# Performance work log

Measured on AMD Instinct MI355X. Metric: run time of the kernel, lower is better.

## Reference

```python
import jax, jax.numpy as jnp
import numpy as np

HEADS = 16
DIM_HEAD = 64
LN_EPS = 1e-5


def setup_inputs() -> dict:
    key = jax.random.key(0)
    ks = jax.random.split(key, 4)
    b, n, dim = 2, 2048, 1024
    inner = HEADS * DIM_HEAD
    x = jax.random.normal(ks[0], (b, n, dim), dtype=jnp.float32)
    gamma = jnp.ones((dim,), dtype=jnp.float32)
    beta = jnp.zeros((dim,), dtype=jnp.float32)
    w_qkv = jax.random.normal(ks[1], (dim, 3 * inner), dtype=jnp.float32) * (dim ** -0.5)
    w_out = jax.random.normal(ks[2], (inner, dim), dtype=jnp.float32) * (inner ** -0.5)
    b_out = jnp.zeros((dim,), dtype=jnp.float32)
    return {"x": x, "gamma": gamma, "beta": beta, "w_qkv": w_qkv, "w_out": w_out, "b_out": b_out}


def reference(x, gamma, beta, w_qkv, w_out, b_out):
    b, n, dim = x.shape
    h, d = HEADS, DIM_HEAD
    scale = d ** -0.5
    # LayerNorm
    mu = jnp.mean(x, axis=-1, keepdims=True)
    var = jnp.mean(jnp.square(x - mu), axis=-1, keepdims=True)
    xn = (x - mu) * jax.lax.rsqrt(var + LN_EPS) * gamma + beta
    # QKV projection (no bias)
    qkv = xn @ w_qkv  # [b, n, 3*h*d]
    q, k, v = jnp.split(qkv, 3, axis=-1)
    split_heads = lambda t: t.reshape(b, n, h, d).transpose(0, 2, 1, 3)  # [b, h, n, d]
    q, k, v = split_heads(q), split_heads(k), split_heads(v)
    q = q * scale
    sim = jnp.einsum('bhid,bhjd->bhij', q, k)  # full O(n^2) score matrix
    attn = jax.nn.softmax(sim, axis=-1)
    out = jnp.einsum('bhij,bhjd->bhid', attn, v)
    out = out.transpose(0, 2, 1, 3).reshape(b, n, h * d)
    return out @ w_out + b_out
```

## Files before the change

kernel.cpp:

```cpp
#include <hip/hip_runtime.h>
#include <hip/hip_bf16.h>

#define HEADS 16
#define DH 64
#define DIM 1024
#define SEQ 2048
#define BATCH 2
#define ROWS (BATCH*SEQ)
#define NQKV (3*DIM)
#define NKVT (SEQ/64)
#define NSPLIT 2
#define QSCALE 0.18033688011112042f
#define NBH (BATCH*HEADS)
#define NQROWS (NBH*SEQ)

typedef __attribute__((ext_vector_type(8))) short bf16x8;
typedef __attribute__((ext_vector_type(4))) float f32x4;
typedef __attribute__((ext_vector_type(16))) float f32x16;
typedef __attribute__((ext_vector_type(4))) unsigned u32x4;
typedef __hip_bfloat16 bf16;

static __device__ __forceinline__ bf16 f2bf(float v){ return __float2bfloat16(v); }

static __device__ __forceinline__ unsigned cvtpk(float a, float b){
  unsigned r;
  asm("v_cvt_pk_bf16_f32 %0, %1, %2" : "=v"(r) : "v"(a), "v"(b));
  return r;
}

static __device__ __forceinline__ void gload16(const void* g, void* lds){
  __builtin_amdgcn_global_load_lds((const __attribute__((address_space(1))) void*)g,
                                   (__attribute__((address_space(3))) void*)lds, 16, 0, 0);
}

__global__ __launch_bounds__(256) void prep_kernel(
    const float* __restrict__ x, const float* __restrict__ gamma,
    const float* __restrict__ beta, bf16* __restrict__ xn,
    const float* __restrict__ w_qkv, bf16* __restrict__ wqt,
    const float* __restrict__ w_out, bf16* __restrict__ wot)
{
  __shared__ float red[8];
  __shared__ __align__(16) bf16 tt[64][72];
  int bid = blockIdx.x;
  int tid = threadIdx.x;
  if (bid < ROWS){
    int row = bid;
    float4 v = ((const float4*)(x + (size_t)row*DIM))[tid];
    float s  = v.x+v.y+v.z+v.w;
    float ss = v.x*v.x+v.y*v.y+v.z*v.z+v.w*v.w;
    #pragma unroll
    for (int m=1;m<64;m<<=1){ s += __shfl_xor(s,m); ss += __shfl_xor(ss,m); }
    int wid = tid>>6;
    if ((tid&63)==0){ red[wid]=s; red[4+wid]=ss; }
    __syncthreads();
    s  = red[0]+red[1]+red[2]+red[3];
    ss = red[4]+red[5]+red[6]+red[7];
    float mu  = s*(1.0f/DIM);
    float var = ss*(1.0f/DIM) - mu*mu;
    float inv = rsqrtf(var + 1e-5f);
    float4 g  = ((const float4*)gamma)[tid];
    float4 bb = ((const float4*)beta)[tid];
    __align__(8) bf16 o[4];
    o[0]=f2bf((v.x-mu)*inv*g.x+bb.x);
    o[1]=f2bf((v.y-mu)*inv*g.y+bb.y);
    o[2]=f2bf((v.z-mu)*inv*g.z+bb.z);
    o[3]=f2bf((v.w-mu)*inv*g.w+bb.w);
    *(uint2*)&xn[(size_t)row*DIM + tid*4] = *(const uint2*)o;
    return;
  }
  const float* in; bf16* out; int R, C, bx, by;
  if (bid < ROWS + 768){
    int idx = bid - ROWS; bx = idx % 48; by = idx / 48;
    in = w_qkv; out = wqt; R = DIM; C = NQKV;
  } else {
    int idx = bid - ROWS - 768; bx = idx % 16; by = idx / 16;
    in = w_out; out = wot; R = DIM; C = DIM;
  }
  int c0 = bx*64, r0 = by*64;
  int row = tid>>2;
  int cq  = (tid&3)*16;
  #pragma unroll
  for (int j=0;j<4;j++){
    float4 v = *(const float4*)&in[(size_t)(r0+row)*C + c0 + cq + j*4];
    tt[cq+j*4+0][row] = f2bf(v.x);
    tt[cq+j*4+1][row] = f2bf(v.y);
    tt[cq+j*4+2][row] = f2bf(v.z);
    tt[cq+j*4+3][row] = f2bf(v.w);
  }
  __syncthreads();
  int c = tid>>2; int rq = (tid&3)*16;
  uint4 u0 = *(const uint4*)&tt[c][rq];
  uint4 u1 = *(const uint4*)&tt[c][rq+8];
  *(uint4*)&out[(size_t)(c0+c)*R + r0 + rq]     = u0;
  *(uint4*)&out[(size_t)(c0+c)*R + r0 + rq + 8] = u1;
}

template<int BM>
__global__ __launch_bounds__(256) void gemm_bt(
    const bf16* __restrict__ A, const bf16* __restrict__ Bt, int K, int mode,
    bf16* __restrict__ qb, bf16* __restrict__ kb, bf16* __restrict__ vtb,
    float* __restrict__ outf, const float* __restrict__ bias)
{
  constexpr int MT = (BM == 128) ? 4 : 2;
  __shared__ __align__(16) bf16 aL[3][BM*32];
  __shared__ __align__(16) bf16 bL[3][128*32];
  int tid = threadIdx.x;
  int w = tid>>6, l = tid&63;
  int lr = l&15, lh = l>>4;
  int wr = w>>1, wc = w&1;
  int by = blockIdx.y, bx = blockIdx.x;
  const bf16* Ab = A  + (size_t)(by*BM)*K;
  const bf16* Bb = Bt + (size_t)(bx*128)*K;
  int srow = w*32 + (l>>2);
  int scol = ((l&3)*8) ^ (((l>>2)&3)<<3);
  int frsw = (lr&3)<<3;
  int nt = K/32;

  f32x4 acc[MT][4] = {};

  auto STAGE = [&](int buf, int k0){
    if constexpr (BM == 128){
      gload16(Ab + (size_t)(srow   )*K + k0 + scol, &aL[buf][w*1024      ]);
      gload16(Ab + (size_t)(srow+16)*K + k0 + scol, &aL[buf][w*1024 + 512]);
    } else {
      gload16(Ab + (size_t)(tid>>2 )*K + k0 + scol, &aL[buf][w*512       ]);
    }
    gload16(Bb + (size_t)(srow   )*K + k0 + scol, &bL[buf][w*1024      ]);
    gload16(Bb + (size_t)(srow+16)*K + k0 + scol, &bL[buf][w*1024 + 512]);
  };

  auto COMPUTE = [&](int buf){
    bf16x8 af[MT], bfr[4];
    #pragma unroll
    for (int m=0;m<MT;m++)
      af[m]  = *(const bf16x8*)&aL[buf][(wr*(MT*16) + m*16 + lr)*32 + ((lh*8) ^ frsw)];
    #pragma unroll
    for (int n=0;n<4;n++)
      bfr[n] = *(const bf16x8*)&bL[buf][(wc*64 + n*16 + lr)*32 + ((lh*8) ^ frsw)];
    #pragma unroll
    for (int m=0;m<MT;m++)
      #pragma unroll
      for (int n=0;n<4;n++)
        acc[m][n] = __builtin_amdgcn_mfma_f32_16x16x32_bf16(af[m], bfr[n], acc[m][n], 0,0,0);
  };

  STAGE(0, 0);
  STAGE(1, 32);
  int cur = 0;
  for (int t=0; t<nt-1; t++){
    if constexpr (BM == 128) asm volatile("s_waitcnt vmcnt(4)" ::: "memory");
    else                     asm volatile("s_waitcnt vmcnt(3)" ::: "memory");
    __builtin_amdgcn_s_barrier();
    __builtin_amdgcn_sched_barrier(0);
    int s2 = cur + 2; if (s2 >= 3) s2 -= 3;
    if (t+2 < nt) STAGE(s2, (t+2)*32);
    COMPUTE(cur);
    cur = (cur == 2) ? 0 : cur + 1;
  }
  asm volatile("s_waitcnt vmcnt(0)" ::: "memory");
  __builtin_amdgcn_s_barrier();
  __builtin_amdgcn_sched_barrier(0);
  COMPUTE(cur);

  int rb = by*BM + wr*(MT*16), cb = bx*128 + wc*64;
  if (mode == 1){
    #pragma unroll
    for (int m=0;m<MT;m++)
      #pragma unroll
      for (int n=0;n<4;n++)
        #pragma unroll
        for (int reg=0;reg<4;reg++){
          int r = rb + m*16 + lh*4 + reg;
          int c = cb + n*16 + lr;
          outf[(size_t)r*DIM + c] = acc[m][n][reg] + bias[c];
        }
  } else if (bx < 8){
    int b = rb >> 11;
    int nn0 = rb & 2047;
    #pragma unroll
    for (int m=0;m<MT;m++)
      #pragma unroll
      for (int n=0;n<4;n++)
        #pragma unroll
        for (int reg=0;reg<4;reg++){
          int nn = nn0 + m*16 + lh*4 + reg;
          int c  = cb + n*16 + lr;
          int hh = c >> 6, dd = c & 63;
          qb[((size_t)(b*HEADS + hh)*SEQ + nn)*DH + dd] = f2bf(acc[m][n][reg]*QSCALE);
        }
  } else if (bx < 16){
    int b = rb >> 11;
    int kvt = (rb & 2047) >> 6;
    int hh0 = ((cb - 1024) >> 6);
    #pragma unroll
    for (int m=0;m<MT;m++)
      #pragma unroll
      for (int reg=0;reg<4;reg++){
        int kvi = m*16 + lh*4 + reg;
        int sw  = (kvi&7)<<3;
        #pragma unroll
        for (int n=0;n<4;n++){
          int dd = n*16 + lr;
          kb[((size_t)(b*HEADS + hh0)*NKVT + kvt)*4096 + kvi*64 + (dd ^ sw)] = f2bf(acc[m][n][reg]);
        }
      }
  } else {
    __syncthreads();
    bf16* tl = (w < 2 ? (bf16*)aL : (bf16*)bL) + (w&1)*4096;
    int b   = rb >> 11;
    int kvt = (rb & 2047) >> 6;
    int hh  = (cb - 2048) >> 6;
    #pragma unroll
    for (int n=0;n<4;n++){
      int dd = n*16 + lr;
      int sw = (dd&7)<<3;
      #pragma unroll
      for (int m=0;m<MT;m++)
        #pragma unroll
        for (int reg=0;reg<4;reg++)
          tl[dd*64 + ((m*16 + lh*4 + reg) ^ sw)] = f2bf(acc[m][n][reg]);
    }
    __syncthreads();
    size_t gb = ((size_t)(b*HEADS + hh)*NKVT + kvt)*4096;
    #pragma unroll
    for (int j=0;j<8;j++)
      *(uint4*)&vtb[gb + j*512 + l*8] = *(const uint4*)&tl[j*512 + l*8];
  }
}

__global__ __launch_bounds__(256,4) void attn_part(
    const bf16* __restrict__ qb, const bf16* __restrict__ kb,
    const bf16* __restrict__ vtb,
    bf16* __restrict__ Opart, float* __restrict__ Mpart, float* __restrict__ Spart)
{
  __shared__ __align__(16) bf16 Kl[2][4096];
  __shared__ __align__(16) bf16 Vl[2][4096];
  int tid = threadIdx.x;
  int w = tid>>6, l = tid&63;
  int q5 = l & 31;
  int hi = l >> 5;
  int swz = (q5&7)<<3;
  int bh = blockIdx.y;
  int sp = blockIdx.z;
  int ts = sp*16, te = ts+16;
  const bf16* Q  = qb  + (size_t)bh*SEQ*DH;
  const bf16* Kt = kb  + (size_t)bh*NKVT*4096;
  const bf16* Vt = vtb + (size_t)bh*NKVT*4096;
  int q0w = blockIdx.x*128 + w*32;

  int co[4];
  #pragma unroll
  for (int st=0;st<4;st++) co[st] = (st*16 + hi*8) ^ swz;
  int r0 = q5*64, r1 = r0 + 2048;

  bf16x8 qf[4];
  #pragma unroll
  for (int st=0;st<4;st++)
    qf[st] = *(const bf16x8*)&Q[(size_t)(q0w + q5)*DH + st*16 + hi*8];

  bf16x8 vone;
  #pragma unroll
  for (int i=0;i<8;i++) vone[i] = (short)0x3f80;

  f32x16 o0 = {}, o1 = {}, osum = {};
  float mrun = -3e38f;

  {
    const bf16* ks = Kt + (size_t)ts*4096;
    const bf16* vs = Vt + (size_t)ts*4096;
    gload16(ks + w*1024       + l*8, &Kl[0][w*1024      ]);
    gload16(ks + w*1024 + 512 + l*8, &Kl[0][w*1024 + 512]);
    gload16(vs + w*1024       + l*8, &Vl[0][w*1024      ]);
    gload16(vs + w*1024 + 512 + l*8, &Vl[0][w*1024 + 512]);
  }

  for (int t=ts; t<te; t++){
    int cur = (t-ts)&1;
    __syncthreads();
    if (t+1 < te){
      const bf16* ks = Kt + (size_t)(t+1)*4096;
      const bf16* vs = Vt + (size_t)(t+1)*4096;
      gload16(ks + w*1024       + l*8, &Kl[cur^1][w*1024      ]);
      gload16(ks + w*1024 + 512 + l*8, &Kl[cur^1][w*1024 + 512]);
      gload16(vs + w*1024       + l*8, &Vl[cur^1][w*1024      ]);
      gload16(vs + w*1024 + 512 + l*8, &Vl[cur^1][w*1024 + 512]);
    }
    f32x16 s0 = {}, s1 = {};
    __builtin_amdgcn_s_setprio(1);
    #pragma unroll
    for (int st=0;st<4;st++){
      bf16x8 kf0 = *(const bf16x8*)&Kl[cur][r0 + co[st]];
      bf16x8 kf1 = *(const bf16x8*)&Kl[cur][r1 + co[st]];
      s0 = __builtin_amdgcn_mfma_f32_32x32x16_bf16(kf0, qf[st], s0, 0,0,0);
      s1 = __builtin_amdgcn_mfma_f32_32x32x16_bf16(kf1, qf[st], s1, 0,0,0);
    }
    __builtin_amdgcn_s_setprio(0);
    float pm = -3e38f;
    #pragma unroll
    for (int r=0;r<16;r++) pm = fmaxf(fmaxf(pm, s0[r]), s1[r]);
    pm = fmaxf(pm, __shfl_xor(pm, 32));
    if (__any(pm > mrun + 8.f)){
      float mn = fmaxf(mrun, pm);
      float sc = __builtin_amdgcn_exp2f(mrun - mn);
      mrun = mn;
      #pragma unroll
      for (int reg=0;reg<16;reg++){
        float scr = __shfl(sc, (l & 32) | ((reg&3) + 8*(reg>>2) + 4*hi));
        o0[reg] *= scr;
        o1[reg] *= scr;
        osum[reg] *= scr;
      }
    }
    #pragma unroll
    for (int r=0;r<16;r++){
      s0[r] = __builtin_amdgcn_exp2f(s0[r] - mrun);
      s1[r] = __builtin_amdgcn_exp2f(s1[r] - mrun);
    }
    #define PV_STEP(SV, SGN, KVS)                                                    \
    {                                                                                \
      unsigned Aw = cvtpk(SV[SGN+0], SV[SGN+1]);                                     \
      unsigned Bw = cvtpk(SV[SGN+2], SV[SGN+3]);                                     \
      unsigned Cw = cvtpk(SV[SGN+4], SV[SGN+5]);                                     \
      unsigned Dw = cvtpk(SV[SGN+6], SV[SGN+7]);                                     \
      asm volatile("v_permlane32_swap_b32 %0, %1" : "+v"(Aw), "+v"(Cw));             \
      asm volatile("v_permlane32_swap_b32 %0, %1" : "+v"(Bw), "+v"(Dw));             \
      u32x4 pw = {Aw, Bw, Cw, Dw};                                                   \
      bf16x8 pa = *(const bf16x8*)&pw;                                               \
      bf16x8 vf0 = *(const bf16x8*)&Vl[cur][r0 + co[KVS]];                           \
      bf16x8 vf1 = *(const bf16x8*)&Vl[cur][r1 + co[KVS]];                           \
      __builtin_amdgcn_s_setprio(1);                                                 \
      o0 = __builtin_amdgcn_mfma_f32_32x32x16_bf16(pa, vf0, o0, 0,0,0);              \
      o1 = __builtin_amdgcn_mfma_f32_32x32x16_bf16(pa, vf1, o1, 0,0,0);              \
      osum = __builtin_amdgcn_mfma_f32_32x32x16_bf16(pa, vone, osum, 0,0,0);         \
      __builtin_amdgcn_s_setprio(0);                                                 \
    }
    PV_STEP(s0, 0, 0)
    PV_STEP(s0, 8, 1)
    PV_STEP(s1, 0, 2)
    PV_STEP(s1, 8, 3)
    #undef PV_STEP
  }
  size_t rbase = ((size_t)sp*NBH + bh)*SEQ;
  #pragma unroll
  for (int reg=0;reg<16;reg++){
    int q = q0w + (reg&3) + 8*(reg>>2) + 4*hi;
    Opart[(rbase + q)*64 + q5]      = f2bf(o0[reg]);
    Opart[(rbase + q)*64 + 32 + q5] = f2bf(o1[reg]);
  }
  if (l < 32)
    Mpart[rbase + q0w + l] = mrun;
  if (q5 == 0){
    #pragma unroll
    for (int reg=0;reg<16;reg++){
      int q = q0w + (reg&3) + 8*(reg>>2) + 4*hi;
      Spart[rbase + q] = osum[reg];
    }
  }
}

__global__ __launch_bounds__(256) void attn_merge(
    const bf16* __restrict__ Opart, const float* __restrict__ Mpart,
    const float* __restrict__ Spart, bf16* __restrict__ ao)
{
  int r = blockIdx.x*4 + (threadIdx.x>>6);
  int d = threadIdx.x & 63;
  float m0 = Mpart[r], m1 = Mpart[NQROWS + r];
  float m  = fmaxf(m0, m1);
  float c0 = exp2f(m0 - m), c1 = exp2f(m1 - m);
  float denom = Spart[r]*c0 + Spart[NQROWS + r]*c1;
  float v = __bfloat162float(Opart[(size_t)r*64 + d])*c0
          + __bfloat162float(Opart[((size_t)NQROWS + r)*64 + d])*c1;
  int bh = r >> 11, q = r & 2047;
  int b = bh >> 4, h = bh & 15;
  ao[((size_t)(b*SEQ + q))*DIM + h*DH + d] = f2bf(v / denom);
}

extern "C" void kernel_launch(void* const* d_in, const int* in_sizes, int n_in,
                              void* d_out, int out_size, void* d_ws, size_t ws_size,
                              hipStream_t stream)
{
  const float* x     = (const float*)d_in[0];
  const float* gamma = (const float*)d_in[1];
  const float* beta  = (const float*)d_in[2];
  const float* w_qkv = (const float*)d_in[3];
  const float* w_out = (const float*)d_in[4];
  const float* b_out = (const float*)d_in[5];
  float* out = (float*)d_out;

  bf16* ws  = (bf16*)d_ws;
  bf16* xn  = ws;
  bf16* wqt = xn  + (size_t)ROWS*DIM;
  bf16* wot = wqt + (size_t)NQKV*DIM;
  bf16* qb  = wot + (size_t)DIM*DIM;
  bf16* kb  = qb  + (size_t)NBH*SEQ*DH;
  bf16* vtb = kb  + (size_t)NBH*SEQ*DH;
  bf16* ao  = vtb + (size_t)NBH*SEQ*DH;
  bf16* Opart = ao + (size_t)ROWS*DIM;
  float* Mpart = (float*)(Opart + (size_t)NSPLIT*NQROWS*DH);
  float* Spart = Mpart + (size_t)NSPLIT*NQROWS;

  prep_kernel<<<dim3(ROWS + 768 + 256), dim3(256), 0, stream>>>(
      x, gamma, beta, xn, w_qkv, wqt, w_out, wot);
  gemm_bt<128><<<dim3(NQKV/128, ROWS/128), dim3(256), 0, stream>>>(
      xn, wqt, DIM, 0, qb, kb, vtb, (float*)nullptr, (const float*)nullptr);
  attn_part<<<dim3(SEQ/128, NBH, NSPLIT), dim3(256), 0, stream>>>(
      qb, kb, vtb, Opart, Mpart, Spart);
  attn_merge<<<dim3(NQROWS/4), dim3(256), 0, stream>>>(Opart, Mpart, Spart, ao);
  gemm_bt<64><<<dim3(DIM/128, ROWS/64), dim3(256), 0, stream>>>(
      ao, wot, DIM, 1, (bf16*)nullptr, (bf16*)nullptr, (bf16*)nullptr, out, b_out);
}
```

Measured before the change: 124.3 us.

## Remap blocks across XCDs and shrink output-projection GEMM tile to 64x64

Adds an XCD-aware linear block remapping to both the GEMM and attention kernels. Consecutive logical tiles, which share A/B rows or the same head's K/V, then land on the same XCD and can reuse its L2. The output-projection GEMM also moves from a 64x128 tile to a square 64x64 tile, which doubles the block count for better CU occupancy on the small N=1024 problem. In exchange, each block loads more operand data per output and pays extra integer index math.

```diff
diff --git a/kernel.cpp b/kernel.cpp
--- a/kernel.cpp
+++ b/kernel.cpp
@@ -102,45 +102,51 @@
     float* __restrict__ outf, const float* __restrict__ bias)
 {
   constexpr int MT = (BM == 128) ? 4 : 2;
+  constexpr int NT = (BM == 128) ? 4 : 2;
   __shared__ __align__(16) bf16 aL[3][BM*32];
-  __shared__ __align__(16) bf16 bL[3][128*32];
+  __shared__ __align__(16) bf16 bL[3][BM*32];
   int tid = threadIdx.x;
   int w = tid>>6, l = tid&63;
   int lr = l&15, lh = l>>4;
   int wr = w>>1, wc = w&1;
-  int by = blockIdx.y, bx = blockIdx.x;
+  int nbx = gridDim.x;
+  int lin = blockIdx.y*nbx + blockIdx.x;
+  int cpx = (nbx*gridDim.y) >> 3;
+  int nl  = (lin & 7)*cpx + (lin >> 3);
+  int bx = nl % nbx, by = nl / nbx;
   const bf16* Ab = A  + (size_t)(by*BM)*K;
-  const bf16* Bb = Bt + (size_t)(bx*128)*K;
+  const bf16* Bb = Bt + (size_t)(bx*BM)*K;
   int srow = w*32 + (l>>2);
   int scol = ((l&3)*8) ^ (((l>>2)&3)<<3);
   int frsw = (lr&3)<<3;
   int nt = K/32;
 
-  f32x4 acc[MT][4] = {};
+  f32x4 acc[MT][NT] = {};
 
   auto STAGE = [&](int buf, int k0){
     if constexpr (BM == 128){
       gload16(Ab + (size_t)(srow   )*K + k0 + scol, &aL[buf][w*1024      ]);
       gload16(Ab + (size_t)(srow+16)*K + k0 + scol, &aL[buf][w*1024 + 512]);
+      gload16(Bb + (size_t)(srow   )*K + k0 + scol, &bL[buf][w*1024      ]);
+      gload16(Bb + (size_t)(srow+16)*K + k0 + scol, &bL[buf][w*1024 + 512]);
     } else {
-      gload16(Ab + (size_t)(tid>>2 )*K + k0 + scol, &aL[buf][w*512       ]);
-    }
-    gload16(Bb + (size_t)(srow   )*K + k0 + scol, &bL[buf][w*1024      ]);
-    gload16(Bb + (size_t)(srow+16)*K + k0 + scol, &bL[buf][w*1024 + 512]);
+      gload16(Ab + (size_t)(tid>>2)*K + k0 + scol, &aL[buf][w*512]);
+      gload16(Bb + (size_t)(tid>>2)*K + k0 + scol, &bL[buf][w*512]);
+    }
   };
 
   auto COMPUTE = [&](int buf){
-    bf16x8 af[MT], bfr[4];
+    bf16x8 af[MT], bfr[NT];
     #pragma unroll
     for (int m=0;m<MT;m++)
       af[m]  = *(const bf16x8*)&aL[buf][(wr*(MT*16) + m*16 + lr)*32 + ((lh*8) ^ frsw)];
     #pragma unroll
-    for (int n=0;n<4;n++)
-      bfr[n] = *(const bf16x8*)&bL[buf][(wc*64 + n*16 + lr)*32 + ((lh*8) ^ frsw)];
+    for (int n=0;n<NT;n++)
+      bfr[n] = *(const bf16x8*)&bL[buf][(wc*(NT*16) + n*16 + lr)*32 + ((lh*8) ^ frsw)];
     #pragma unroll
     for (int m=0;m<MT;m++)
       #pragma unroll
-      for (int n=0;n<4;n++)
+      for (int n=0;n<NT;n++)
         acc[m][n] = __builtin_amdgcn_mfma_f32_16x16x32_bf16(af[m], bfr[n], acc[m][n], 0,0,0);
   };
 
@@ -149,7 +155,7 @@
   int cur = 0;
   for (int t=0; t<nt-1; t++){
     if constexpr (BM == 128) asm volatile("s_waitcnt vmcnt(4)" ::: "memory");
-    else                     asm volatile("s_waitcnt vmcnt(3)" ::: "memory");
+    else                     asm volatile("s_waitcnt vmcnt(2)" ::: "memory");
     __builtin_amdgcn_s_barrier();
     __builtin_amdgcn_sched_barrier(0);
     int s2 = cur + 2; if (s2 >= 3) s2 -= 3;
@@ -162,12 +168,12 @@
   __builtin_amdgcn_sched_barrier(0);
   COMPUTE(cur);
 
-  int rb = by*BM + wr*(MT*16), cb = bx*128 + wc*64;
+  int rb = by*BM + wr*(MT*16), cb = bx*BM + wc*(NT*16);
   if (mode == 1){
     #pragma unroll
     for (int m=0;m<MT;m++)
       #pragma unroll
-      for (int n=0;n<4;n++)
+      for (int n=0;n<NT;n++)
         #pragma unroll
         for (int reg=0;reg<4;reg++){
           int r = rb + m*16 + lh*4 + reg;
@@ -180,7 +186,7 @@
     #pragma unroll
     for (int m=0;m<MT;m++)
       #pragma unroll
-      for (int n=0;n<4;n++)
+      for (int n=0;n<NT;n++)
         #pragma unroll
         for (int reg=0;reg<4;reg++){
           int nn = nn0 + m*16 + lh*4 + reg;
@@ -199,7 +205,7 @@
         int kvi = m*16 + lh*4 + reg;
         int sw  = (kvi&7)<<3;
         #pragma unroll
-        for (int n=0;n<4;n++){
+        for (int n=0;n<NT;n++){
           int dd = n*16 + lr;
           kb[((size_t)(b*HEADS + hh0)*NKVT + kvt)*4096 + kvi*64 + (dd ^ sw)] = f2bf(acc[m][n][reg]);
         }
@@ -211,7 +217,7 @@
     int kvt = (rb & 2047) >> 6;
     int hh  = (cb - 2048) >> 6;
     #pragma unroll
-    for (int n=0;n<4;n++){
+    for (int n=0;n<NT;n++){
       int dd = n*16 + lr;
       int sw = (dd&7)<<3;
       #pragma unroll
@@ -240,13 +246,16 @@
   int q5 = l & 31;
   int hi = l >> 5;
   int swz = (q5&7)<<3;
-  int bh = blockIdx.y;
-  int sp = blockIdx.z;
+  int lin = (blockIdx.z*gridDim.y + blockIdx.y)*gridDim.x + blockIdx.x;
+  int nl  = (lin & 7)*128 + (lin >> 3);
+  int bqx = nl & 15;
+  int bh  = (nl >> 4) & 31;
+  int sp  = nl >> 9;
   int ts = sp*16, te = ts+16;
   const bf16* Q  = qb  + (size_t)bh*SEQ*DH;
   const bf16* Kt = kb  + (size_t)bh*NKVT*4096;
   const bf16* Vt = vtb + (size_t)bh*NKVT*4096;
-  int q0w = blockIdx.x*128 + w*32;
+  int q0w = bqx*128 + w*32;
 
   int co[4];
   #pragma unroll
@@ -406,6 +415,6 @@
   attn_part<<<dim3(SEQ/128, NBH, NSPLIT), dim3(256), 0, stream>>>(
       qb, kb, vtb, Opart, Mpart, Spart);
   attn_merge<<<dim3(NQROWS/4), dim3(256), 0, stream>>>(Opart, Mpart, Spart, ao);
-  gemm_bt<64><<<dim3(DIM/128, ROWS/64), dim3(256), 0, stream>>>(
+  gemm_bt<64><<<dim3(DIM/64, ROWS/64), dim3(256), 0, stream>>>(
       ao, wot, DIM, 1, (bf16*)nullptr, (bf16*)nullptr, (bf16*)nullptr, out, b_out);
 }
```

Result: no change. 122.8 us (median of 2 runs) (-1.2%).
